# Performance work log

Measured on AMD Instinct MI355X. Metric: run time of the kernel, lower is better.

## Reference

```python
import jax, jax.numpy as jnp
import numpy as np

N = 100000        # nodes in the batched graph
E = 1_600_000     # directed edges
G = 256           # graphs in the batch
IN, H = 3, 64
EPS = 1e-5        # BatchNorm eps (eval mode: running stats, dropout off)


def setup_inputs() -> dict:
    key = jax.random.key(0)
    ks = jax.random.split(key, 40)
    inp = {}
    inp["x"] = jax.random.normal(ks[0], (N, IN), jnp.float32)
    inp["edge_index"] = jax.random.randint(ks[1], (2, E), 0, N, dtype=jnp.int32)
    inp["batch_idx"] = jnp.sort(jax.random.randint(ks[2], (N,), 0, G, dtype=jnp.int32))
    dims = [IN, H, H, H]  # zip(dims[:-1], dims[1:]) -> 3 GCN layers (as in source)
    k = 3
    for i in range(3):
        inp[f"W{i}"] = jax.random.normal(ks[k], (dims[i], dims[i + 1]), jnp.float32) * 0.1; k += 1
        inp[f"b{i}"] = jax.random.normal(ks[k], (dims[i + 1],), jnp.float32) * 0.01; k += 1
        inp[f"g{i}"] = jax.random.uniform(ks[k], (dims[i + 1],), jnp.float32, 0.5, 1.5); k += 1
        inp[f"be{i}"] = jax.random.normal(ks[k], (dims[i + 1],), jnp.float32) * 0.1; k += 1
        inp[f"rm{i}"] = jax.random.normal(ks[k], (dims[i + 1],), jnp.float32) * 0.1; k += 1
        inp[f"rv{i}"] = jax.random.uniform(ks[k], (dims[i + 1],), jnp.float32, 0.5, 1.5); k += 1
    inp["mW1"] = jax.random.normal(ks[k], (2 * H, 32), jnp.float32) * 0.1; k += 1
    inp["mb1"] = jnp.zeros((32,), jnp.float32)
    inp["mW2"] = jax.random.normal(ks[k], (32, 16), jnp.float32) * 0.1; k += 1
    inp["mb2"] = jnp.zeros((16,), jnp.float32)
    inp["mW3"] = jax.random.normal(ks[k], (16, 1), jnp.float32) * 0.1; k += 1
    inp["mb3"] = jnp.zeros((1,), jnp.float32)
    return inp


def _gcn(x, W, b, src, dst):
    # PyG GCNConv: add self-loops, symmetric D^-1/2 (A+I) D^-1/2 normalization
    h = x @ W                                   # [N, out]
    deg = jnp.zeros((N,), h.dtype).at[dst].add(1.0) + 1.0  # +1 self-loop
    dinv = jax.lax.rsqrt(deg)
    coef = dinv[src] * dinv[dst]                # [E]
    agg = jax.ops.segment_sum(h[src] * coef[:, None], dst, num_segments=N)
    agg = agg + h * (dinv * dinv)[:, None]      # self-loop message
    return agg + b


def _bn(x, g, be, rm, rv):
    return (x - rm) * jax.lax.rsqrt(rv + EPS) * g + be


def _forward(x, edge_index, batch_idx,
             W0, b0, g0, be0, rm0, rv0,
             W1, b1, g1, be1, rm1, rv1,
             W2, b2, g2, be2, rm2, rv2,
             mW1, mb1, mW2, mb2, mW3, mb3):
    src, dst = edge_index[0], edge_index[1]
    layers = [(W0, b0, g0, be0, rm0, rv0), (W1, b1, g1, be1, rm1, rv1), (W2, b2, g2, be2, rm2, rv2)]
    for (W, b, g, be, rm, rv) in layers:
        x = jax.nn.relu(_bn(_gcn(x, W, b, src, dst), g, be, rm, rv))
    cnt = jax.ops.segment_sum(jnp.ones((N,), x.dtype), batch_idx, num_segments=G)
    x_mean = jax.ops.segment_sum(x, batch_idx, num_segments=G) / jnp.maximum(cnt, 1.0)[:, None]
    x_max = jax.ops.segment_max(x, batch_idx, num_segments=G)
    x_max = jnp.where(jnp.isfinite(x_max), x_max, 0.0)
    xg = jnp.concatenate([x_mean, x_max], axis=1)  # [G, 2H]
    h = jax.nn.relu(xg @ mW1 + mb1)
    h = jax.nn.relu(h @ mW2 + mb2)
    return h @ mW3 + mb3                            # [G, 1]


def reference(x, edge_index, batch_idx,
              W0, b0, g0, be0, rm0, rv0,
              W1, b1, g1, be1, rm1, rv1,
              W2, b2, g2, be2, rm2, rv2,
              mW1, mb1, mW2, mb2, mW3, mb3):
    return _forward(x, edge_index, batch_idx,
                    W0, b0, g0, be0, rm0, rv0,
                    W1, b1, g1, be1, rm1, rv1,
                    W2, b2, g2, be2, rm2, rv2,
                    mW1, mb1, mW2, mb2, mW3, mb3)
```

## Files before the change

### kernel.cpp

```cpp
#include <hip/hip_runtime.h>
#include <hip/hip_fp16.h>

#define NN 100000
#define EE 1600000
#define GG 256
#define EPS 1e-5f
#define KB2 ((NN + 511) >> 9)
#define BCAP 10240
#define EPB 4096
#define EBLK ((EE + EPB - 1) / EPB)
#define NB256 ((NN + 255) / 256)

__device__ __forceinline__ unsigned int pack2(float x, float y) {
  __half2 h = __float22half2_rn(make_float2(x, y));
  return *reinterpret_cast<unsigned int*>(&h);
}
__device__ __forceinline__ uint2 pack4(float x, float y, float z, float w) {
  uint2 r;
  r.x = pack2(x, y);
  r.y = pack2(z, w);
  return r;
}
__device__ __forceinline__ void add8(float4& a0, float4& a1, uint4 v) {
  __half2 h0 = *reinterpret_cast<__half2*>(&v.x);
  __half2 h1 = *reinterpret_cast<__half2*>(&v.y);
  __half2 h2 = *reinterpret_cast<__half2*>(&v.z);
  __half2 h3 = *reinterpret_cast<__half2*>(&v.w);
  float2 f0 = __half22float2(h0), f1 = __half22float2(h1);
  float2 f2 = __half22float2(h2), f3 = __half22float2(h3);
  a0.x += f0.x; a0.y += f0.y; a0.z += f1.x; a0.w += f1.y;
  a1.x += f2.x; a1.y += f2.y; a1.z += f3.x; a1.w += f3.y;
}

__device__ __forceinline__ void gld16(uint4& d, const uint4* p) {
  asm volatile("global_load_dwordx4 %0, %1, off" : "=v"(d) : "v"(p));
}
__device__ __forceinline__ void gldf16(float4& d, const float4* p) {
  asm volatile("global_load_dwordx4 %0, %1, off" : "=v"(d) : "v"(p));
}
__device__ __forceinline__ void gld4(int& d, const int* p) {
  asm volatile("global_load_dword %0, %1, off" : "=v"(d) : "v"(p));
}

__global__ void k_passA(const int* __restrict__ ei, int* __restrict__ bfill,
                        int* __restrict__ tmp) {
  __shared__ int cnt[KB2], cur[KB2], base[KB2];
  int t = threadIdx.x;
  for (int b = t; b < KB2; b += 256) { cnt[b] = 0; cur[b] = 0; }
  __syncthreads();
  int e0 = blockIdx.x * EPB;
  int myb[16], myp[16];
#pragma unroll
  for (int j = 0; j < 16; ++j) {
    int e = e0 + j * 256 + t;
    int bb = -1, pp = 0;
    if (e < EE) {
      int ss = ei[e];
      int dd = ei[EE + e];
      bb = dd >> 9;
      pp = (ss << 9) | (dd & 511);
    }
    myb[j] = bb;
    myp[j] = pp;
    if (bb >= 0) atomicAdd(&cnt[bb], 1);
  }
  __syncthreads();
  for (int b = t; b < KB2; b += 256)
    if (cnt[b] > 0) base[b] = b * BCAP + atomicAdd(&bfill[b], cnt[b]);
  __syncthreads();
#pragma unroll
  for (int j = 0; j < 16; ++j) {
    int bb = myb[j];
    if (bb >= 0) {
      int slot = base[bb] + atomicAdd(&cur[bb], 1);
      tmp[slot] = myp[j];
    }
  }
}

__global__ void k_bucket(const int* __restrict__ tmp, const int* __restrict__ bfill,
                         const float* __restrict__ x, int* __restrict__ csr,
                         int* __restrict__ row, int* __restrict__ rowe,
                         float* __restrict__ dinv, float4* __restrict__ xd) {
  __shared__ int cnt[512], s[512], fillp[512];
  __shared__ int stmp[BCAP];
  int b = blockIdx.x, t = threadIdx.x;
  int nb = b << 9;
  int e0 = b * BCAP;
  int fill = bfill[b];
  cnt[t] = 0;
  cnt[t + 256] = 0;
  for (int e = t; e < fill; e += 256) stmp[e] = tmp[e0 + e];
  __syncthreads();
  for (int e = t; e < fill; e += 256) atomicAdd(&cnt[stmp[e] & 511], 1);
  __syncthreads();
  s[t] = cnt[t];
  s[t + 256] = cnt[t + 256];
  __syncthreads();
  for (int off = 1; off < 512; off <<= 1) {
    int i1 = t + 256;
    int v0 = (t >= off) ? s[t - off] : 0;
    int v1 = (i1 >= off) ? s[i1 - off] : 0;
    __syncthreads();
    s[t] += v0;
    s[i1] += v1;
    __syncthreads();
  }
#pragma unroll
  for (int k = 0; k < 2; ++k) {
    int i = t + k * 256;
    int excl = s[i] - cnt[i];
    fillp[i] = excl;
    int dst = nb + i;
    if (dst < NN) {
      row[dst] = e0 + excl;
      rowe[dst] = e0 + s[i];
      float d = rsqrtf((float)cnt[i] + 1.0f);
      dinv[dst] = d;
      xd[dst] = make_float4(x[dst * 3] * d, x[dst * 3 + 1] * d, x[dst * 3 + 2] * d, 0.f);
    }
  }
  __syncthreads();
  for (int e = t; e < fill; e += 256) {
    int ed = stmp[e];
    int slot = atomicAdd(&fillp[ed & 511], 1);
    csr[e0 + slot] = ed >> 9;
  }
}

__launch_bounds__(256, 4)
__global__ void k_agg3f(const float4* __restrict__ xd, const int* __restrict__ row,
                        const int* __restrict__ rowe, const int* __restrict__ csr,
                        const float* __restrict__ dinv,
                        const float* __restrict__ W, const float* __restrict__ b,
                        const float* __restrict__ gam, const float* __restrict__ bet,
                        const float* __restrict__ rm, const float* __restrict__ rv,
                        uint2* __restrict__ out) {
  int n = blockIdx.x * 256 + threadIdx.x;
  if (n >= NN) return;
  int s0 = row[n], s1 = rowe[n];
  float4 a = xd[n];
  float ax = a.x, ay = a.y, az = a.z;
  for (int i = s0; i < s1; i += 16) {
    int idx[16];
#pragma unroll
    for (int j = 0; j < 16; ++j) gld4(idx[j], csr + min(i + j, s1 - 1));
    asm volatile("s_waitcnt vmcnt(0)" ::: "memory");
    __builtin_amdgcn_sched_barrier(0);
    float4 v[16];
#pragma unroll
    for (int j = 0; j < 16; ++j) gldf16(v[j], xd + idx[j]);
    asm volatile("s_waitcnt vmcnt(0)" ::: "memory");
    __builtin_amdgcn_sched_barrier(0);
    int rem = s1 - i;
#pragma unroll
    for (int j = 0; j < 16; ++j)
      if (j < rem) { ax += v[j].x; ay += v[j].y; az += v[j].z; }
  }
  float d = dinv[n];
  float t0 = ax * d, t1 = ay * d, t2 = az * d;
  const float4* W4 = (const float4*)W;
  const float4* b4 = (const float4*)b;
  const float4* g4p = (const float4*)gam;
  const float4* be4p = (const float4*)bet;
  const float4* rm4p = (const float4*)rm;
  const float4* rv4p = (const float4*)rv;
#pragma unroll
  for (int c4 = 0; c4 < 16; ++c4) {
    float4 w0 = W4[c4], w1 = W4[16 + c4], w2 = W4[32 + c4];
    float4 bb = b4[c4], g4 = g4p[c4], be4 = be4p[c4], rm4 = rm4p[c4], rv4 = rv4p[c4];
    float4 o;
    o.x = fmaf(t0, w0.x, fmaf(t1, w1.x, fmaf(t2, w2.x, bb.x)));
    o.y = fmaf(t0, w0.y, fmaf(t1, w1.y, fmaf(t2, w2.y, bb.y)));
    o.z = fmaf(t0, w0.z, fmaf(t1, w1.z, fmaf(t2, w2.z, bb.z)));
    o.w = fmaf(t0, w0.w, fmaf(t1, w1.w, fmaf(t2, w2.w, bb.w)));
    float scx = g4.x * rsqrtf(rv4.x + EPS), shx = be4.x - rm4.x * scx;
    float scy = g4.y * rsqrtf(rv4.y + EPS), shy = be4.y - rm4.y * scy;
    float scz = g4.z * rsqrtf(rv4.z + EPS), shz = be4.z - rm4.z * scz;
    float scw = g4.w * rsqrtf(rv4.w + EPS), shw = be4.w - rm4.w * scw;
    o.x = fmaxf(fmaf(o.x, scx, shx), 0.f) * d;
    o.y = fmaxf(fmaf(o.y, scy, shy), 0.f) * d;
    o.z = fmaxf(fmaf(o.z, scz, shz), 0.f) * d;
    o.w = fmaxf(fmaf(o.w, scw, shw), 0.f) * d;
    out[(size_t)n * 16 + c4] = pack4(o.x, o.y, o.z, o.w);
  }
}

template <bool MID>
__launch_bounds__(256, 4)
__global__ void k_layer2(const uint4* __restrict__ xs, const int* __restrict__ row,
                         const int* __restrict__ rowe, const int* __restrict__ csr,
                         const float* __restrict__ dinv,
                         const float* __restrict__ W, const float* __restrict__ b,
                         const float* __restrict__ gam, const float* __restrict__ bet,
                         const float* __restrict__ rm, const float* __restrict__ rv,
                         void* __restrict__ outv) {
  __shared__ float sh[32][68];
  int t = blockIdx.x * 256 + threadIdx.x;
  int n = t >> 3, sub = t & 7;
  int local = threadIdx.x >> 3;
  int s0 = row[n], s1 = rowe[n];
  float4 a0 = make_float4(0.f, 0.f, 0.f, 0.f);
  float4 a1 = make_float4(0.f, 0.f, 0.f, 0.f);
  add8(a0, a1, xs[(size_t)n * 8 + sub]);
  if (s0 < s1) {
    int e = s0 + sub;
    int myidx = (e < s1) ? csr[e] : n;
    for (int i = s0; i < s1; i += 8) {
      int e2 = i + 8 + sub;
      int pre;
      gld4(pre, csr + min(e2, s1 - 1));
      uint4 v0, v1, v2, v3, v4, v5, v6, v7;
      gld16(v0, xs + ((size_t)__shfl(myidx, 0, 8) * 8 + sub));
      gld16(v1, xs + ((size_t)__shfl(myidx, 1, 8) * 8 + sub));
      gld16(v2, xs + ((size_t)__shfl(myidx, 2, 8) * 8 + sub));
      gld16(v3, xs + ((size_t)__shfl(myidx, 3, 8) * 8 + sub));
      gld16(v4, xs + ((size_t)__shfl(myidx, 4, 8) * 8 + sub));
      gld16(v5, xs + ((size_t)__shfl(myidx, 5, 8) * 8 + sub));
      gld16(v6, xs + ((size_t)__shfl(myidx, 6, 8) * 8 + sub));
      gld16(v7, xs + ((size_t)__shfl(myidx, 7, 8) * 8 + sub));
      asm volatile("s_waitcnt vmcnt(0)" ::: "memory");
      __builtin_amdgcn_sched_barrier(0);
      int rem = s1 - i;
      add8(a0, a1, v0);
      if (rem > 1) add8(a0, a1, v1);
      if (rem > 2) add8(a0, a1, v2);
      if (rem > 3) add8(a0, a1, v3);
      if (rem > 4) add8(a0, a1, v4);
      if (rem > 5) add8(a0, a1, v5);
      if (rem > 6) add8(a0, a1, v6);
      if (rem > 7) add8(a0, a1, v7);
      myidx = (e2 < s1) ? pre : n;
    }
  }
  float d = dinv[n];
  float4 w0 = make_float4(a0.x * d, a0.y * d, a0.z * d, a0.w * d);
  float4 w1 = make_float4(a1.x * d, a1.y * d, a1.z * d, a1.w * d);
  *(float4*)&sh[local][sub * 8] = w0;
  *(float4*)&sh[local][sub * 8 + 4] = w1;
  __syncthreads();
  const float4* W4 = (const float4*)W;
  float4 accA = ((const float4*)b)[sub * 2];
  float4 accB = ((const float4*)b)[sub * 2 + 1];
#pragma unroll 8
  for (int k = 0; k < 64; ++k) {
    float xv = sh[local][k];
    float4 wA = W4[k * 16 + sub * 2];
    float4 wB = W4[k * 16 + sub * 2 + 1];
    accA.x = fmaf(xv, wA.x, accA.x);
    accA.y = fmaf(xv, wA.y, accA.y);
    accA.z = fmaf(xv, wA.z, accA.z);
    accA.w = fmaf(xv, wA.w, accA.w);
    accB.x = fmaf(xv, wB.x, accB.x);
    accB.y = fmaf(xv, wB.y, accB.y);
    accB.z = fmaf(xv, wB.z, accB.z);
    accB.w = fmaf(xv, wB.w, accB.w);
  }
  float4 gA = ((const float4*)gam)[sub * 2], gB = ((const float4*)gam)[sub * 2 + 1];
  float4 beA = ((const float4*)bet)[sub * 2], beB = ((const float4*)bet)[sub * 2 + 1];
  float4 rmA = ((const float4*)rm)[sub * 2], rmB = ((const float4*)rm)[sub * 2 + 1];
  float4 rvA = ((const float4*)rv)[sub * 2], rvB = ((const float4*)rv)[sub * 2 + 1];
  float4 oA, oB;
  {
    float sc = gA.x * rsqrtf(rvA.x + EPS); oA.x = fmaxf(fmaf(accA.x, sc, beA.x - rmA.x * sc), 0.f);
    sc = gA.y * rsqrtf(rvA.y + EPS); oA.y = fmaxf(fmaf(accA.y, sc, beA.y - rmA.y * sc), 0.f);
    sc = gA.z * rsqrtf(rvA.z + EPS); oA.z = fmaxf(fmaf(accA.z, sc, beA.z - rmA.z * sc), 0.f);
    sc = gA.w * rsqrtf(rvA.w + EPS); oA.w = fmaxf(fmaf(accA.w, sc, beA.w - rmA.w * sc), 0.f);
    sc = gB.x * rsqrtf(rvB.x + EPS); oB.x = fmaxf(fmaf(accB.x, sc, beB.x - rmB.x * sc), 0.f);
    sc = gB.y * rsqrtf(rvB.y + EPS); oB.y = fmaxf(fmaf(accB.y, sc, beB.y - rmB.y * sc), 0.f);
    sc = gB.z * rsqrtf(rvB.z + EPS); oB.z = fmaxf(fmaf(accB.z, sc, beB.z - rmB.z * sc), 0.f);
    sc = gB.w * rsqrtf(rvB.w + EPS); oB.w = fmaxf(fmaf(accB.w, sc, beB.w - rmB.w * sc), 0.f);
  }
  if (MID) {
    uint4 r;
    r.x = pack2(oA.x * d, oA.y * d);
    r.y = pack2(oA.z * d, oA.w * d);
    r.z = pack2(oB.x * d, oB.y * d);
    r.w = pack2(oB.z * d, oB.w * d);
    ((uint4*)outv)[(size_t)n * 8 + sub] = r;
  } else {
    ((float4*)outv)[(size_t)n * 16 + sub * 2] = oA;
    ((float4*)outv)[(size_t)n * 16 + sub * 2 + 1] = oB;
  }
}

__device__ __forceinline__ int lower_bound(const int* __restrict__ b, int target) {
  int lo = 0, hi = NN;
  while (lo < hi) {
    int m = (lo + hi) >> 1;
    if (b[m] < target) lo = m + 1; else hi = m;
  }
  return lo;
}

__global__ void k_poolmlp(const float4* __restrict__ feat, const int* __restrict__ bidx,
                          const float* __restrict__ mW1, const float* __restrict__ mb1,
                          const float* __restrict__ mW2, const float* __restrict__ mb2,
                          const float* __restrict__ mW3, const float* __restrict__ mb3,
                          float* __restrict__ out) {
  __shared__ float4 shs[64][17], shm[64][17];
  __shared__ float xg[128], h1[32], h2[16];
  int g = blockIdx.x, t = threadIdx.x;
  int c4 = t & 15, r = t >> 4;
  int lo = lower_bound(bidx, g);
  int hi = lower_bound(bidx, g + 1);
  float4 s = make_float4(0.f, 0.f, 0.f, 0.f);
  float4 m = make_float4(0.f, 0.f, 0.f, 0.f);
  for (int i = lo + r; i < hi; i += 64) {
    float4 v = feat[(size_t)i * 16 + c4];
    s.x += v.x; s.y += v.y; s.z += v.z; s.w += v.w;
    m.x = fmaxf(m.x, v.x); m.y = fmaxf(m.y, v.y);
    m.z = fmaxf(m.z, v.z); m.w = fmaxf(m.w, v.w);
  }
  shs[r][c4] = s;
  shm[r][c4] = m;
  __syncthreads();
  if (t < 16) {
    float4 cs = shs[0][t], cm = shm[0][t];
#pragma unroll
    for (int r2 = 1; r2 < 64; ++r2) {
      float4 as = shs[r2][t], am = shm[r2][t];
      cs.x += as.x; cs.y += as.y; cs.z += as.z; cs.w += as.w;
      cm.x = fmaxf(cm.x, am.x); cm.y = fmaxf(cm.y, am.y);
      cm.z = fmaxf(cm.z, am.z); cm.w = fmaxf(cm.w, am.w);
    }
    float inv = 1.0f / fmaxf((float)(hi - lo), 1.0f);
    xg[t * 4 + 0] = cs.x * inv; xg[t * 4 + 1] = cs.y * inv;
    xg[t * 4 + 2] = cs.z * inv; xg[t * 4 + 3] = cs.w * inv;
    xg[64 + t * 4 + 0] = cm.x; xg[64 + t * 4 + 1] = cm.y;
    xg[64 + t * 4 + 2] = cm.z; xg[64 + t * 4 + 3] = cm.w;
  }
  __syncthreads();
  if (t < 32) {
    float a = mb1[t];
    for (int k = 0; k < 128; ++k) a = fmaf(xg[k], mW1[k * 32 + t], a);
    h1[t] = fmaxf(a, 0.f);
  }
  __syncthreads();
  if (t < 16) {
    float a = mb2[t];
    for (int k = 0; k < 32; ++k) a = fmaf(h1[k], mW2[k * 16 + t], a);
    h2[t] = fmaxf(a, 0.f);
  }
  __syncthreads();
  if (t == 0) {
    float a = mb3[0];
    for (int k = 0; k < 16; ++k) a = fmaf(h2[k], mW3[k], a);
    out[g] = a;
  }
}

extern "C" void kernel_launch(void* const* d_in, const int* in_sizes, int n_in,
                              void* d_out, int out_size, void* d_ws, size_t ws_size,
                              hipStream_t stream) {
  const float* x = (const float*)d_in[0];
  const int* ei = (const int*)d_in[1];
  const int* bidx = (const int*)d_in[2];
  const float *W[3], *b[3], *gam[3], *bet[3], *rm[3], *rv[3];
  for (int l = 0; l < 3; ++l) {
    W[l] = (const float*)d_in[3 + 6 * l];
    b[l] = (const float*)d_in[4 + 6 * l];
    gam[l] = (const float*)d_in[5 + 6 * l];
    bet[l] = (const float*)d_in[6 + 6 * l];
    rm[l] = (const float*)d_in[7 + 6 * l];
    rv[l] = (const float*)d_in[8 + 6 * l];
  }
  const float* mW1 = (const float*)d_in[21];
  const float* mb1 = (const float*)d_in[22];
  const float* mW2 = (const float*)d_in[23];
  const float* mb2 = (const float*)d_in[24];
  const float* mW3 = (const float*)d_in[25];
  const float* mb3 = (const float*)d_in[26];
  float* out = (float*)d_out;

  char* ws = (char*)d_ws;
  size_t off = 0;
  auto alloc = [&](size_t bytes) {
    void* p = ws + off;
    off = (off + bytes + 1023) & ~(size_t)1023;
    return p;
  };
  float* dinv = (float*)alloc(NN * 4);
  int* row = (int*)alloc(NN * 4);
  int* rowe = (int*)alloc(NN * 4);
  int* csr = (int*)alloc((size_t)KB2 * BCAP * 4);
  int* bfill = (int*)alloc(256 * 4);
  float4* xd = (float4*)alloc((size_t)NN * 16);
  float* bufA = (float*)alloc((size_t)NN * 64 * 4);
  float* bufB = (float*)alloc((size_t)NN * 64 * 2);
  int* tmp = (int*)bufA;

  hipMemsetAsync(bfill, 0, 256 * 4, stream);

  k_passA<<<EBLK, 256, 0, stream>>>(ei, bfill, tmp);
  k_bucket<<<KB2, 256, 0, stream>>>(tmp, bfill, x, csr, row, rowe, dinv, xd);

  int nb8 = (NN * 8) / 256;

  k_agg3f<<<NB256, 256, 0, stream>>>(xd, row, rowe, csr, dinv, W[0], b[0], gam[0], bet[0],
                                     rm[0], rv[0], (uint2*)bufA);
  k_layer2<true><<<nb8, 256, 0, stream>>>((const uint4*)bufA, row, rowe, csr, dinv, W[1], b[1],
                                          gam[1], bet[1], rm[1], rv[1], (void*)bufB);
  k_layer2<false><<<nb8, 256, 0, stream>>>((const uint4*)bufB, row, rowe, csr, dinv, W[2], b[2],
                                           gam[2], bet[2], rm[2], rv[2], (void*)bufA);
  k_poolmlp<<<GG, 1024, 0, stream>>>((const float4*)bufA, bidx, mW1, mb1, mW2, mb2, mW3, mb3, out);
}
```

Baseline: 323.8 us.

## Use nontemporal loads/stores and store final layer features as fp16

Replaces streaming global loads and stores across the preprocessing and layer kernels with nontemporal builtins, and removes the explicit waitcnt/sched_barrier after index loads in the first-layer aggregation. The last GCN layer now writes half-precision features (8 bytes per 4 channels instead of 16), and the pooling kernel reads and converts fp16. This cuts memory traffic for the final feature buffer and tries to reduce cache pollution, at the cost of fp16 rounding on the pooled features. Nontemporal hints on data that is reused (csr, xs gathers) could hurt cache hit rates.

```diff
diff --git a/kernel.cpp b/kernel.cpp
--- a/kernel.cpp
+++ b/kernel.cpp
@@ -11,6 +11,26 @@
 #define EBLK ((EE + EPB - 1) / EPB)
 #define NB256 ((NN + 255) / 256)
 
+typedef unsigned int vuint4 __attribute__((ext_vector_type(4)));
+typedef unsigned int vuint2 __attribute__((ext_vector_type(2)));
+typedef float vfloat4 __attribute__((ext_vector_type(4)));
+
+__device__ __forceinline__ int ntl4(const int* p) { return __builtin_nontemporal_load(p); }
+__device__ __forceinline__ float ntlf(const float* p) { return __builtin_nontemporal_load(p); }
+__device__ __forceinline__ uint2 ntl8(const uint2* p) {
+  vuint2 w = __builtin_nontemporal_load((const vuint2*)p);
+  return make_uint2(w.x, w.y);
+}
+__device__ __forceinline__ void nts4(int* p, int v) { __builtin_nontemporal_store(v, p); }
+__device__ __forceinline__ void nts16u(uint4* p, uint4 v) {
+  vuint4 w = {v.x, v.y, v.z, v.w};
+  __builtin_nontemporal_store(w, (vuint4*)p);
+}
+__device__ __forceinline__ void nts8u(uint2* p, uint2 v) {
+  vuint2 w = {v.x, v.y};
+  __builtin_nontemporal_store(w, (vuint2*)p);
+}
+
 __device__ __forceinline__ unsigned int pack2(float x, float y) {
   __half2 h = __float22half2_rn(make_float2(x, y));
   return *reinterpret_cast<unsigned int*>(&h);
@@ -38,9 +58,6 @@
 __device__ __forceinline__ void gldf16(float4& d, const float4* p) {
   asm volatile("global_load_dwordx4 %0, %1, off" : "=v"(d) : "v"(p));
 }
-__device__ __forceinline__ void gld4(int& d, const int* p) {
-  asm volatile("global_load_dword %0, %1, off" : "=v"(d) : "v"(p));
-}
 
 __global__ void k_passA(const int* __restrict__ ei, int* __restrict__ bfill,
                         int* __restrict__ tmp) {
@@ -55,8 +72,8 @@
     int e = e0 + j * 256 + t;
     int bb = -1, pp = 0;
     if (e < EE) {
-      int ss = ei[e];
-      int dd = ei[EE + e];
+      int ss = ntl4(ei + e);
+      int dd = ntl4(ei + EE + e);
       bb = dd >> 9;
       pp = (ss << 9) | (dd & 511);
     }
@@ -73,7 +90,7 @@
     int bb = myb[j];
     if (bb >= 0) {
       int slot = base[bb] + atomicAdd(&cur[bb], 1);
-      tmp[slot] = myp[j];
+      nts4(tmp + slot, myp[j]);
     }
   }
 }
@@ -90,7 +107,7 @@
   int fill = bfill[b];
   cnt[t] = 0;
   cnt[t + 256] = 0;
-  for (int e = t; e < fill; e += 256) stmp[e] = tmp[e0 + e];
+  for (int e = t; e < fill; e += 256) stmp[e] = ntl4(tmp + e0 + e);
   __syncthreads();
   for (int e = t; e < fill; e += 256) atomicAdd(&cnt[stmp[e] & 511], 1);
   __syncthreads();
@@ -117,14 +134,15 @@
       rowe[dst] = e0 + s[i];
       float d = rsqrtf((float)cnt[i] + 1.0f);
       dinv[dst] = d;
-      xd[dst] = make_float4(x[dst * 3] * d, x[dst * 3 + 1] * d, x[dst * 3 + 2] * d, 0.f);
+      xd[dst] = make_float4(ntlf(x + dst * 3) * d, ntlf(x + dst * 3 + 1) * d,
+                            ntlf(x + dst * 3 + 2) * d, 0.f);
     }
   }
   __syncthreads();
   for (int e = t; e < fill; e += 256) {
     int ed = stmp[e];
     int slot = atomicAdd(&fillp[ed & 511], 1);
-    csr[e0 + slot] = ed >> 9;
+    nts4(csr + e0 + slot, ed >> 9);
   }
 }
 
@@ -144,9 +162,7 @@
   for (int i = s0; i < s1; i += 16) {
     int idx[16];
 #pragma unroll
-    for (int j = 0; j < 16; ++j) gld4(idx[j], csr + min(i + j, s1 - 1));
-    asm volatile("s_waitcnt vmcnt(0)" ::: "memory");
-    __builtin_amdgcn_sched_barrier(0);
+    for (int j = 0; j < 16; ++j) idx[j] = ntl4(csr + min(i + j, s1 - 1));
     float4 v[16];
 #pragma unroll
     for (int j = 0; j < 16; ++j) gldf16(v[j], xd + idx[j]);
@@ -182,7 +198,7 @@
     o.y = fmaxf(fmaf(o.y, scy, shy), 0.f) * d;
     o.z = fmaxf(fmaf(o.z, scz, shz), 0.f) * d;
     o.w = fmaxf(fmaf(o.w, scw, shw), 0.f) * d;
-    out[(size_t)n * 16 + c4] = pack4(o.x, o.y, o.z, o.w);
+    nts8u(out + (size_t)n * 16 + c4, pack4(o.x, o.y, o.z, o.w));
   }
 }
 
@@ -194,7 +210,7 @@
                          const float* __restrict__ W, const float* __restrict__ b,
                          const float* __restrict__ gam, const float* __restrict__ bet,
                          const float* __restrict__ rm, const float* __restrict__ rv,
-                         void* __restrict__ outv) {
+                         uint4* __restrict__ outv) {
   __shared__ float sh[32][68];
   int t = blockIdx.x * 256 + threadIdx.x;
   int n = t >> 3, sub = t & 7;
@@ -205,11 +221,10 @@
   add8(a0, a1, xs[(size_t)n * 8 + sub]);
   if (s0 < s1) {
     int e = s0 + sub;
-    int myidx = (e < s1) ? csr[e] : n;
+    int myidx = (e < s1) ? ntl4(csr + e) : n;
     for (int i = s0; i < s1; i += 8) {
       int e2 = i + 8 + sub;
-      int pre;
-      gld4(pre, csr + min(e2, s1 - 1));
+      int pre = ntl4(csr + min(e2, s1 - 1));
       uint4 v0, v1, v2, v3, v4, v5, v6, v7;
       gld16(v0, xs + ((size_t)__shfl(myidx, 0, 8) * 8 + sub));
       gld16(v1, xs + ((size_t)__shfl(myidx, 1, 8) * 8 + sub));
@@ -271,17 +286,19 @@
     sc = gB.z * rsqrtf(rvB.z + EPS); oB.z = fmaxf(fmaf(accB.z, sc, beB.z - rmB.z * sc), 0.f);
     sc = gB.w * rsqrtf(rvB.w + EPS); oB.w = fmaxf(fmaf(accB.w, sc, beB.w - rmB.w * sc), 0.f);
   }
+  uint4 r;
   if (MID) {
-    uint4 r;
     r.x = pack2(oA.x * d, oA.y * d);
     r.y = pack2(oA.z * d, oA.w * d);
     r.z = pack2(oB.x * d, oB.y * d);
     r.w = pack2(oB.z * d, oB.w * d);
-    ((uint4*)outv)[(size_t)n * 8 + sub] = r;
   } else {
-    ((float4*)outv)[(size_t)n * 16 + sub * 2] = oA;
-    ((float4*)outv)[(size_t)n * 16 + sub * 2 + 1] = oB;
-  }
+    r.x = pack2(oA.x, oA.y);
+    r.y = pack2(oA.z, oA.w);
+    r.z = pack2(oB.x, oB.y);
+    r.w = pack2(oB.z, oB.w);
+  }
+  nts16u(outv + (size_t)n * 8 + sub, r);
 }
 
 __device__ __forceinline__ int lower_bound(const int* __restrict__ b, int target) {
@@ -293,7 +310,7 @@
   return lo;
 }
 
-__global__ void k_poolmlp(const float4* __restrict__ feat, const int* __restrict__ bidx,
+__global__ void k_poolmlp(const uint2* __restrict__ feat, const int* __restrict__ bidx,
                           const float* __restrict__ mW1, const float* __restrict__ mb1,
                           const float* __restrict__ mW2, const float* __restrict__ mb2,
                           const float* __restrict__ mW3, const float* __restrict__ mb3,
@@ -307,10 +324,13 @@
   float4 s = make_float4(0.f, 0.f, 0.f, 0.f);
   float4 m = make_float4(0.f, 0.f, 0.f, 0.f);
   for (int i = lo + r; i < hi; i += 64) {
-    float4 v = feat[(size_t)i * 16 + c4];
-    s.x += v.x; s.y += v.y; s.z += v.z; s.w += v.w;
-    m.x = fmaxf(m.x, v.x); m.y = fmaxf(m.y, v.y);
-    m.z = fmaxf(m.z, v.z); m.w = fmaxf(m.w, v.w);
+    uint2 u = ntl8(feat + (size_t)i * 16 + c4);
+    __half2 h0 = *reinterpret_cast<__half2*>(&u.x);
+    __half2 h1v = *reinterpret_cast<__half2*>(&u.y);
+    float2 f0 = __half22float2(h0), f1 = __half22float2(h1v);
+    s.x += f0.x; s.y += f0.y; s.z += f1.x; s.w += f1.y;
+    m.x = fmaxf(m.x, f0.x); m.y = fmaxf(m.y, f0.y);
+    m.z = fmaxf(m.z, f1.x); m.w = fmaxf(m.w, f1.y);
   }
   shs[r][c4] = s;
   shm[r][c4] = m;
@@ -400,8 +420,8 @@
   k_agg3f<<<NB256, 256, 0, stream>>>(xd, row, rowe, csr, dinv, W[0], b[0], gam[0], bet[0],
                                      rm[0], rv[0], (uint2*)bufA);
   k_layer2<true><<<nb8, 256, 0, stream>>>((const uint4*)bufA, row, rowe, csr, dinv, W[1], b[1],
-                                          gam[1], bet[1], rm[1], rv[1], (void*)bufB);
+                                          gam[1], bet[1], rm[1], rv[1], (uint4*)bufB);
   k_layer2<false><<<nb8, 256, 0, stream>>>((const uint4*)bufB, row, rowe, csr, dinv, W[2], b[2],
-                                           gam[2], bet[2], rm[2], rv[2], (void*)bufA);
-  k_poolmlp<<<GG, 1024, 0, stream>>>((const float4*)bufA, bidx, mW1, mb1, mW2, mb2, mW3, mb3, out);
-}
+                                           gam[2], bet[2], rm[2], rv[2], (uint4*)bufA);
+  k_poolmlp<<<GG, 1024, 0, stream>>>((const uint2*)bufA, bidx, mW1, mb1, mW2, mb2, mW3, mb3, out);
+}
```

Measured after the change: 407.3 us. 1.26x slower.

## Store final layer output in fp16 and drop manual index-load asm

Applied to the files above, without the earlier changes.

The last GCN layer now writes its 64-channel output as packed fp16 instead of fp32, and the pooling kernel reads and widens that fp16 data. This halves the write and read traffic of the final activation buffer at the cost of fp16 rounding before pooling. Separately, the inline-asm index loads with explicit waitcnt and sched barriers in the layer-1 and layer-2 gathers are replaced with plain C++ loads, leaving scheduling to the compiler.

```diff
diff --git a/kernel.cpp b/kernel.cpp
--- a/kernel.cpp
+++ b/kernel.cpp
@@ -37,9 +37,6 @@
 }
 __device__ __forceinline__ void gldf16(float4& d, const float4* p) {
   asm volatile("global_load_dwordx4 %0, %1, off" : "=v"(d) : "v"(p));
-}
-__device__ __forceinline__ void gld4(int& d, const int* p) {
-  asm volatile("global_load_dword %0, %1, off" : "=v"(d) : "v"(p));
 }
 
 __global__ void k_passA(const int* __restrict__ ei, int* __restrict__ bfill,
@@ -144,9 +141,7 @@
   for (int i = s0; i < s1; i += 16) {
     int idx[16];
 #pragma unroll
-    for (int j = 0; j < 16; ++j) gld4(idx[j], csr + min(i + j, s1 - 1));
-    asm volatile("s_waitcnt vmcnt(0)" ::: "memory");
-    __builtin_amdgcn_sched_barrier(0);
+    for (int j = 0; j < 16; ++j) idx[j] = csr[min(i + j, s1 - 1)];
     float4 v[16];
 #pragma unroll
     for (int j = 0; j < 16; ++j) gldf16(v[j], xd + idx[j]);
@@ -194,7 +189,7 @@
                          const float* __restrict__ W, const float* __restrict__ b,
                          const float* __restrict__ gam, const float* __restrict__ bet,
                          const float* __restrict__ rm, const float* __restrict__ rv,
-                         void* __restrict__ outv) {
+                         uint4* __restrict__ outv) {
   __shared__ float sh[32][68];
   int t = blockIdx.x * 256 + threadIdx.x;
   int n = t >> 3, sub = t & 7;
@@ -208,8 +203,7 @@
     int myidx = (e < s1) ? csr[e] : n;
     for (int i = s0; i < s1; i += 8) {
       int e2 = i + 8 + sub;
-      int pre;
-      gld4(pre, csr + min(e2, s1 - 1));
+      int pre = csr[min(e2, s1 - 1)];
       uint4 v0, v1, v2, v3, v4, v5, v6, v7;
       gld16(v0, xs + ((size_t)__shfl(myidx, 0, 8) * 8 + sub));
       gld16(v1, xs + ((size_t)__shfl(myidx, 1, 8) * 8 + sub));
@@ -271,17 +265,19 @@
     sc = gB.z * rsqrtf(rvB.z + EPS); oB.z = fmaxf(fmaf(accB.z, sc, beB.z - rmB.z * sc), 0.f);
     sc = gB.w * rsqrtf(rvB.w + EPS); oB.w = fmaxf(fmaf(accB.w, sc, beB.w - rmB.w * sc), 0.f);
   }
+  uint4 r;
   if (MID) {
-    uint4 r;
     r.x = pack2(oA.x * d, oA.y * d);
     r.y = pack2(oA.z * d, oA.w * d);
     r.z = pack2(oB.x * d, oB.y * d);
     r.w = pack2(oB.z * d, oB.w * d);
-    ((uint4*)outv)[(size_t)n * 8 + sub] = r;
   } else {
-    ((float4*)outv)[(size_t)n * 16 + sub * 2] = oA;
-    ((float4*)outv)[(size_t)n * 16 + sub * 2 + 1] = oB;
-  }
+    r.x = pack2(oA.x, oA.y);
+    r.y = pack2(oA.z, oA.w);
+    r.z = pack2(oB.x, oB.y);
+    r.w = pack2(oB.z, oB.w);
+  }
+  outv[(size_t)n * 8 + sub] = r;
 }
 
 __device__ __forceinline__ int lower_bound(const int* __restrict__ b, int target) {
@@ -293,7 +289,7 @@
   return lo;
 }
 
-__global__ void k_poolmlp(const float4* __restrict__ feat, const int* __restrict__ bidx,
+__global__ void k_poolmlp(const uint2* __restrict__ feat, const int* __restrict__ bidx,
                           const float* __restrict__ mW1, const float* __restrict__ mb1,
                           const float* __restrict__ mW2, const float* __restrict__ mb2,
                           const float* __restrict__ mW3, const float* __restrict__ mb3,
@@ -307,10 +303,13 @@
   float4 s = make_float4(0.f, 0.f, 0.f, 0.f);
   float4 m = make_float4(0.f, 0.f, 0.f, 0.f);
   for (int i = lo + r; i < hi; i += 64) {
-    float4 v = feat[(size_t)i * 16 + c4];
-    s.x += v.x; s.y += v.y; s.z += v.z; s.w += v.w;
-    m.x = fmaxf(m.x, v.x); m.y = fmaxf(m.y, v.y);
-    m.z = fmaxf(m.z, v.z); m.w = fmaxf(m.w, v.w);
+    uint2 u = feat[(size_t)i * 16 + c4];
+    __half2 h0 = *reinterpret_cast<__half2*>(&u.x);
+    __half2 h1v = *reinterpret_cast<__half2*>(&u.y);
+    float2 f0 = __half22float2(h0), f1 = __half22float2(h1v);
+    s.x += f0.x; s.y += f0.y; s.z += f1.x; s.w += f1.y;
+    m.x = fmaxf(m.x, f0.x); m.y = fmaxf(m.y, f0.y);
+    m.z = fmaxf(m.z, f1.x); m.w = fmaxf(m.w, f1.y);
   }
   shs[r][c4] = s;
   shm[r][c4] = m;
@@ -400,8 +399,8 @@
   k_agg3f<<<NB256, 256, 0, stream>>>(xd, row, rowe, csr, dinv, W[0], b[0], gam[0], bet[0],
                                      rm[0], rv[0], (uint2*)bufA);
   k_layer2<true><<<nb8, 256, 0, stream>>>((const uint4*)bufA, row, rowe, csr, dinv, W[1], b[1],
-                                          gam[1], bet[1], rm[1], rv[1], (void*)bufB);
+                                          gam[1], bet[1], rm[1], rv[1], (uint4*)bufB);
   k_layer2<false><<<nb8, 256, 0, stream>>>((const uint4*)bufB, row, rowe, csr, dinv, W[2], b[2],
-                                           gam[2], bet[2], rm[2], rv[2], (void*)bufA);
-  k_poolmlp<<<GG, 1024, 0, stream>>>((const float4*)bufA, bidx, mW1, mb1, mW2, mb2, mW3, mb3, out);
-}
+                                           gam[2], bet[2], rm[2], rv[2], (uint4*)bufA);
+  k_poolmlp<<<GG, 1024, 0, stream>>>((const uint2*)bufA, bidx, mW1, mb1, mW2, mb2, mW3, mb3, out);
+}
```

Result: no change. 320.5 us (-1.0%).
